# Performance work log

Hardware: AMD Instinct MI355X
Metric: run time of the kernel (lower is better)

## Reference

```python
import jax, jax.numpy as jnp
import numpy as np

DIM = 1024
N_HEADS = 16
HEAD_DIM = DIM // N_HEADS


def setup_inputs() -> dict:
    key = jax.random.key(0)
    k_x, k_wqkv, k_bqkv, k_wp, k_bp = jax.random.split(key, 5)
    s = 1.0 / np.sqrt(DIM)
    return {
        "x": jax.random.normal(k_x, (2, 2048, DIM), dtype=jnp.float32),
        "w_qkv": jax.random.uniform(k_wqkv, (3 * DIM, DIM), minval=-s, maxval=s, dtype=jnp.float32),
        "b_qkv": jax.random.uniform(k_bqkv, (3 * DIM,), minval=-s, maxval=s, dtype=jnp.float32),
        "w_proj": jax.random.uniform(k_wp, (DIM, DIM), minval=-s, maxval=s, dtype=jnp.float32),
        "b_proj": jax.random.uniform(k_bp, (DIM,), minval=-s, maxval=s, dtype=jnp.float32),
    }


def reference(x, w_qkv, b_qkv, w_proj, b_proj):
    B, S, D = x.shape
    H, Hd = N_HEADS, HEAD_DIM
    scale = jnp.asarray(Hd, x.dtype) ** 0.5
    qkv = x @ w_qkv.T + b_qkv                      # [B, S, 3D]
    q, k, v = jnp.split(qkv, 3, axis=-1)
    # [B, S, D] -> [B, H, S, Hd]
    q = q.reshape(B, S, H, Hd).transpose(0, 2, 1, 3)
    k = k.reshape(B, S, H, Hd).transpose(0, 2, 1, 3)
    v = v.reshape(B, S, H, Hd).transpose(0, 2, 1, 3)
    attn = jnp.einsum("bhqd,bhkd->bhqk", q, k) / scale
    attn = jax.nn.softmax(attn, axis=-1)
    out = jnp.einsum("bhqk,bhkd->bhqd", attn, v)   # [B, H, S, Hd]
    out = out.transpose(0, 2, 1, 3).reshape(B, S, D)
    return out @ w_proj.T + b_proj
```

## Files before the change

### kernel.cpp

```cpp
#include <hip/hip_runtime.h>

typedef __bf16 bf16;
typedef __bf16 bf16x4 __attribute__((ext_vector_type(4)));
typedef __bf16 bf16x8 __attribute__((ext_vector_type(8)));
typedef float f32x4 __attribute__((ext_vector_type(4)));
typedef float f32x16 __attribute__((ext_vector_type(16)));

#define DIMD 1024
#define NHEAD 16
#define HDIM 64
#define BATCH 2
#define SEQ 2048
#define MTOT (BATCH*SEQ)

#define EXP2F(x) __builtin_amdgcn_exp2f(x)

#define OFF_XB (0ull)
#define OFF_OB (0ull)
#define OFF_VT (8ull<<20)
#define OFF_WP (8ull<<20)

__device__ __forceinline__ void g2l16(const void* g, void* l) {
  __builtin_amdgcn_global_load_lds(
      (const __attribute__((address_space(1))) void*)g,
      (__attribute__((address_space(3))) void*)l,
      16, 0, 0);
}

__device__ __forceinline__ bf16x8 cvt8(float4 a, float4 b) {
  bf16x8 r = { (bf16)a.x, (bf16)a.y, (bf16)a.z, (bf16)a.w,
               (bf16)b.x, (bf16)b.y, (bf16)b.z, (bf16)b.w };
  return r;
}

__global__ __launch_bounds__(256) void cvt_kernel(const float* __restrict__ in,
                                                  bf16* __restrict__ out, int n4) {
  int i = blockIdx.x * blockDim.x + threadIdx.x;
  if (i < n4) {
    float4 v = ((const float4*)in)[i];
    bf16x4 o = { (bf16)v.x, (bf16)v.y, (bf16)v.z, (bf16)v.w };
    ((bf16x4*)out)[i] = o;
  }
}

__global__ __launch_bounds__(256, 3) void gemm_qkv(
    const bf16* __restrict__ A, const float* __restrict__ W,
    const float* __restrict__ bias,
    bf16* __restrict__ Qb, bf16* __restrict__ Kb, bf16* __restrict__ Vt)
{
  __shared__ bf16 lA[2][128 * 32];
  __shared__ bf16 lB[2][128 * 32];
  const int tid = threadIdx.x;
  const int wave = tid >> 6, lane = tid & 63;
  const int l15 = lane & 15, quad = lane >> 4;
  const int wm = wave >> 1, wn = wave & 1;
  const int tm = blockIdx.y * 128, tn = blockIdx.x * 128;

  f32x4 acc[4][4] = {};

  const int srow = tid >> 2, sch = (tid & 3) * 8;
  const bf16*  ga = &A[(size_t)(tm + srow) * DIMD + sch];
  const float* gb = &W[(size_t)(tn + srow) * DIMD + sch];

  g2l16(ga,                     &lA[0][wave * 512]);
  g2l16(ga + (size_t)64 * DIMD, &lA[0][2048 + wave * 512]);
  float4 bv0 = ((const float4*)gb)[0], bv1 = ((const float4*)gb)[1];
  float4 bv2 = ((const float4*)(gb + (size_t)64 * DIMD))[0],
         bv3 = ((const float4*)(gb + (size_t)64 * DIMD))[1];

  for (int kt = 0; kt < 32; kt++) {
    bf16* sB = lB[kt & 1];
    *(bf16x8*)&sB[srow * 32 + sch]        = cvt8(bv0, bv1);
    *(bf16x8*)&sB[(64 + srow) * 32 + sch] = cvt8(bv2, bv3);
    __syncthreads();

    if (kt < 31) {
      const int kn = (kt + 1) * 32;
      bf16* nA = lA[(kt + 1) & 1];
      g2l16(ga + kn,                     &nA[wave * 512]);
      g2l16(ga + kn + (size_t)64 * DIMD, &nA[2048 + wave * 512]);
      const float* gbn = gb + kn;
      bv0 = ((const float4*)gbn)[0]; bv1 = ((const float4*)gbn)[1];
      bv2 = ((const float4*)(gbn + (size_t)64 * DIMD))[0];
      bv3 = ((const float4*)(gbn + (size_t)64 * DIMD))[1];
    }

    const bf16* sA = lA[kt & 1];
    bf16x8 af[4], bfr[4];
#pragma unroll
    for (int i = 0; i < 4; i++)
      af[i] = *(const bf16x8*)&sA[(wm * 64 + i * 16 + l15) * 32 + quad * 8];
#pragma unroll
    for (int i = 0; i < 4; i++)
      bfr[i] = *(const bf16x8*)&sB[(wn * 64 + i * 16 + l15) * 32 + quad * 8];
#pragma unroll
    for (int i = 0; i < 4; i++)
#pragma unroll
      for (int j = 0; j < 4; j++)
        acc[i][j] = __builtin_amdgcn_mfma_f32_16x16x32_bf16(af[i], bfr[j], acc[i][j], 0, 0, 0);
  }

  const int sel = tn >> 10;
#pragma unroll
  for (int j = 0; j < 4; j++) {
    const int n = tn + wn * 64 + j * 16 + l15;
    const float bv = bias[n];
    const int d = n & 1023, h = d >> 6, hd = d & 63;
#pragma unroll
    for (int i = 0; i < 4; i++) {
      const int mbase = tm + wm * 64 + i * 16 + quad * 4;
      const int b = mbase >> 11, s0 = mbase & 2047;
      const int bh = b * NHEAD + h;
      if (sel == 2) {
        bf16x4 vv = { (bf16)(acc[i][j][0] + bv), (bf16)(acc[i][j][1] + bv),
                      (bf16)(acc[i][j][2] + bv), (bf16)(acc[i][j][3] + bv) };
        *(bf16x4*)&Vt[((size_t)bh * HDIM + hd) * SEQ + s0] = vv;
      } else {
#pragma unroll
        for (int r = 0; r < 4; r++) {
          float v = acc[i][j][r] + bv;
          if (sel == 0)
            Qb[((size_t)bh * SEQ + s0 + r) * HDIM + hd] = (bf16)(v * 0.18033688f);
          else
            Kb[((size_t)bh * SEQ + s0 + r) * HDIM + hd] = (bf16)v;
        }
      }
    }
  }
}

__global__ __launch_bounds__(256, 2) void gemm_proj(
    const bf16* __restrict__ A, const bf16* __restrict__ Bt,
    const float* __restrict__ bias, float* __restrict__ out)
{
  __shared__ bf16 lA[2][64 * 32];
  __shared__ bf16 lB[2][128 * 32];
  const int tid = threadIdx.x;
  const int wave = tid >> 6, lane = tid & 63;
  const int l15 = lane & 15, quad = lane >> 4;
  const int tm = blockIdx.y * 64, tn = blockIdx.x * 128;

  f32x4 acc[4][2] = {};

  const int srow = tid >> 2, sch = (tid & 3) * 8;
  const bf16* ga = &A[(size_t)(tm + srow) * DIMD + sch];
  const bf16* gb = &Bt[(size_t)(tn + srow) * DIMD + sch];

  g2l16(ga,                     &lA[0][wave * 512]);
  g2l16(gb,                     &lB[0][wave * 512]);
  g2l16(gb + (size_t)64 * DIMD, &lB[0][2048 + wave * 512]);

  for (int kt = 0; kt < 32; kt++) {
    __syncthreads();

    if (kt < 31) {
      const int kn = (kt + 1) * 32;
      bf16* nA = lA[(kt + 1) & 1];
      bf16* nB = lB[(kt + 1) & 1];
      g2l16(ga + kn,                     &nA[wave * 512]);
      g2l16(gb + kn,                     &nB[wave * 512]);
      g2l16(gb + kn + (size_t)64 * DIMD, &nB[2048 + wave * 512]);
    }

    const bf16* sA = lA[kt & 1];
    const bf16* sB = lB[kt & 1];
    bf16x8 af[4], bfr[2];
#pragma unroll
    for (int i = 0; i < 4; i++)
      af[i] = *(const bf16x8*)&sA[(i * 16 + l15) * 32 + quad * 8];
#pragma unroll
    for (int j = 0; j < 2; j++)
      bfr[j] = *(const bf16x8*)&sB[(wave * 32 + j * 16 + l15) * 32 + quad * 8];
#pragma unroll
    for (int i = 0; i < 4; i++)
#pragma unroll
      for (int j = 0; j < 2; j++)
        acc[i][j] = __builtin_amdgcn_mfma_f32_16x16x32_bf16(af[i], bfr[j], acc[i][j], 0, 0, 0);
  }

#pragma unroll
  for (int j = 0; j < 2; j++) {
    const int n = tn + wave * 32 + j * 16 + l15;
    const float bv = bias[n];
#pragma unroll
    for (int i = 0; i < 4; i++) {
      const int mbase = tm + i * 16 + quad * 4;
#pragma unroll
      for (int r = 0; r < 4; r++)
        out[(size_t)(mbase + r) * DIMD + n] = acc[i][j][r] + bv;
    }
  }
}

#define LSTR 72
__global__ __launch_bounds__(256, 2) void attn_kernel(
    const bf16* __restrict__ Qb, const bf16* __restrict__ Kb,
    const bf16* __restrict__ Vt, bf16* __restrict__ Ob)
{
  __shared__ bf16 lKV[2][2][64 * LSTR];
  __shared__ bf16 lP[4][32 * LSTR];

  const int tid = threadIdx.x;
  const int wave = tid >> 6, lane = tid & 63;
  const int l31 = lane & 31, h = lane >> 5;
  const int xcd = blockIdx.x & 7, grp = blockIdx.x >> 3;
  const int bh = xcd + 8 * (grp & 3);
  const int qt = grp >> 2;

  const int qrow = qt * 128 + wave * 32 + l31;
  const bf16* qp = Qb + ((size_t)bh * SEQ + qrow) * HDIM + h * 8;
  bf16x8 qf[4];
#pragma unroll
  for (int c = 0; c < 4; c++) qf[c] = *(const bf16x8*)(qp + c * 16);

  const int srow = tid >> 3;
  const int sch = (tid & 7) * 8;
  const bf16* kg = Kb + ((size_t)bh * SEQ + srow) * HDIM + sch;
  const bf16* vg = Vt + ((size_t)bh * HDIM + srow) * SEQ + sch;

  uint4 kr0 = *(const uint4*)(kg);
  uint4 kr1 = *(const uint4*)(kg + 32 * HDIM);
  uint4 vr0 = *(const uint4*)(vg);
  uint4 vr1 = *(const uint4*)(vg + 32 * SEQ);

  bf16* pw = lP[wave];

  f32x16 o0 = {}, o1 = {};
  float mrow = -1e30f, lrow = 0.f;

  for (int kt = 0; kt < SEQ / 64; kt++) {
    bf16* sK = lKV[kt & 1][0];
    bf16* sV = lKV[kt & 1][1];
    *(uint4*)&sK[srow * LSTR + sch]        = kr0;
    *(uint4*)&sK[(32 + srow) * LSTR + sch] = kr1;
    *(uint4*)&sV[srow * LSTR + sch]        = vr0;
    *(uint4*)&sV[(32 + srow) * LSTR + sch] = vr1;
    __syncthreads();

    const int ktn = (kt + 1) & (SEQ / 64 - 1);
    kr0 = *(const uint4*)(kg + (size_t)ktn * 64 * HDIM);
    kr1 = *(const uint4*)(kg + (size_t)ktn * 64 * HDIM + 32 * HDIM);
    vr0 = *(const uint4*)(vg + ktn * 64);
    vr1 = *(const uint4*)(vg + ktn * 64 + 32 * SEQ);

    f32x16 s0 = {}, s1 = {};
#pragma unroll
    for (int c = 0; c < 4; c++) {
      bf16x8 k0 = *(const bf16x8*)&sK[l31 * LSTR + c * 16 + h * 8];
      bf16x8 k1 = *(const bf16x8*)&sK[(32 + l31) * LSTR + c * 16 + h * 8];
      s0 = __builtin_amdgcn_mfma_f32_32x32x16_bf16(k0, qf[c], s0, 0, 0, 0);
      s1 = __builtin_amdgcn_mfma_f32_32x32x16_bf16(k1, qf[c], s1, 0, 0, 0);
    }

    if (kt > 0) {
      const bf16* pV = lKV[(kt + 1) & 1][1];
#pragma unroll
      for (int c = 0; c < 4; c++) {
        bf16x8 pf = *(const bf16x8*)&pw[l31 * LSTR + c * 16 + h * 8];
        bf16x8 v0 = *(const bf16x8*)&pV[l31 * LSTR + c * 16 + h * 8];
        bf16x8 v1 = *(const bf16x8*)&pV[(32 + l31) * LSTR + c * 16 + h * 8];
        o0 = __builtin_amdgcn_mfma_f32_32x32x16_bf16(v0, pf, o0, 0, 0, 0);
        o1 = __builtin_amdgcn_mfma_f32_32x32x16_bf16(v1, pf, o1, 0, 0, 0);
      }
    }

    float mx = -1e30f;
#pragma unroll
    for (int r = 0; r < 16; r++) { mx = fmaxf(mx, s0[r]); mx = fmaxf(mx, s1[r]); }
    mx = fmaxf(mx, __shfl_xor(mx, 32, 64));
    const float nm = fmaxf(mrow, mx);
    const float alpha = EXP2F(mrow - nm);
    mrow = nm;

    float rs = 0.f;
#pragma unroll
    for (int r = 0; r < 16; r++) {
      const float p0 = EXP2F(s0[r] - nm);
      const float p1 = EXP2F(s1[r] - nm);
      s0[r] = p0; s1[r] = p1;
      rs += p0 + p1;
    }
    rs += __shfl_xor(rs, 32, 64);
    lrow = lrow * alpha + rs;

#pragma unroll
    for (int r = 0; r < 16; r++) { o0[r] *= alpha; o1[r] *= alpha; }

#pragma unroll
    for (int g = 0; g < 4; g++) {
      bf16x4 pa = { (bf16)s0[4*g], (bf16)s0[4*g+1], (bf16)s0[4*g+2], (bf16)s0[4*g+3] };
      bf16x4 pb = { (bf16)s1[4*g], (bf16)s1[4*g+1], (bf16)s1[4*g+2], (bf16)s1[4*g+3] };
      *(bf16x4*)&pw[l31 * LSTR + g * 8 + h * 4]      = pa;
      *(bf16x4*)&pw[l31 * LSTR + 32 + g * 8 + h * 4] = pb;
    }
  }

  {
    const bf16* pV = lKV[1][1];
#pragma unroll
    for (int c = 0; c < 4; c++) {
      bf16x8 pf = *(const bf16x8*)&pw[l31 * LSTR + c * 16 + h * 8];
      bf16x8 v0 = *(const bf16x8*)&pV[l31 * LSTR + c * 16 + h * 8];
      bf16x8 v1 = *(const bf16x8*)&pV[(32 + l31) * LSTR + c * 16 + h * 8];
      o0 = __builtin_amdgcn_mfma_f32_32x32x16_bf16(v0, pf, o0, 0, 0, 0);
      o1 = __builtin_amdgcn_mfma_f32_32x32x16_bf16(v1, pf, o1, 0, 0, 0);
    }
  }

  const int b = bh >> 4, head = bh & 15;
  const float inv = 1.f / lrow;
  const size_t base = ((size_t)b * SEQ + qrow) * DIMD + head * HDIM;
#pragma unroll
  for (int g = 0; g < 4; g++) {
    bf16x4 oa = { (bf16)(o0[4*g] * inv), (bf16)(o0[4*g+1] * inv),
                  (bf16)(o0[4*g+2] * inv), (bf16)(o0[4*g+3] * inv) };
    bf16x4 ob = { (bf16)(o1[4*g] * inv), (bf16)(o1[4*g+1] * inv),
                  (bf16)(o1[4*g+2] * inv), (bf16)(o1[4*g+3] * inv) };
    *(bf16x4*)&Ob[base + g * 8 + h * 4]      = oa;
    *(bf16x4*)&Ob[base + 32 + g * 8 + h * 4] = ob;
  }
}

extern "C" void kernel_launch(void* const* d_in, const int* in_sizes, int n_in,
                              void* d_out, int out_size, void* d_ws, size_t ws_size,
                              hipStream_t stream) {
  const float* x      = (const float*)d_in[0];
  const float* w_qkv  = (const float*)d_in[1];
  const float* b_qkv  = (const float*)d_in[2];
  const float* w_proj = (const float*)d_in[3];
  const float* b_proj = (const float*)d_in[4];
  float* out = (float*)d_out;
  char* ws = (char*)d_ws;

  bf16* Qb = (bf16*)d_out;
  bf16* Kb = (bf16*)d_out + (size_t)MTOT * DIMD;
  bf16* xb     = (bf16*)(ws + OFF_XB);
  bf16* Ob     = (bf16*)(ws + OFF_OB);
  bf16* Vt     = (bf16*)(ws + OFF_VT);
  bf16* wprojb = (bf16*)(ws + OFF_WP);

  cvt_kernel<<<(MTOT * DIMD / 4) / 256, 256, 0, stream>>>(x, xb, MTOT * DIMD / 4);
  gemm_qkv<<<dim3(24, 32), 256, 0, stream>>>(xb, w_qkv, b_qkv, Qb, Kb, Vt);
  attn_kernel<<<BATCH * NHEAD * (SEQ / 128), 256, 0, stream>>>(Qb, Kb, Vt, Ob);
  cvt_kernel<<<(DIMD * DIMD / 4) / 256, 256, 0, stream>>>(w_proj, wprojb, DIMD * DIMD / 4);
  gemm_proj<<<dim3(8, 64), 256, 0, stream>>>(Ob, wprojb, b_proj, out);
}
```

Baseline: 194.5 us.

## Load V fragments directly to registers, swizzle LDS, add lazy softmax rescale

The attention kernel stops staging V in shared memory. Each lane now loads its V^T MFMA fragments straight from global memory into registers one iteration ahead. K and P tiles move from padded LDS rows to an XOR-swizzled 128-byte layout to avoid bank conflicts, and MFMA sections are wrapped in s_setprio. Softmax rescaling is skipped unless the running max grows by more than 8 (log2 units), and the max and sum reductions become trees. This cuts LDS traffic and exp/multiply work but raises register pressure and global load latency exposure, and it may lose precision when rescaling is deferred.

```diff
diff --git a/kernel.cpp b/kernel.cpp
--- a/kernel.cpp
+++ b/kernel.cpp
@@ -192,13 +192,12 @@
   }
 }
 
-#define LSTR 72
 __global__ __launch_bounds__(256, 2) void attn_kernel(
     const bf16* __restrict__ Qb, const bf16* __restrict__ Kb,
     const bf16* __restrict__ Vt, bf16* __restrict__ Ob)
 {
-  __shared__ bf16 lKV[2][2][64 * LSTR];
-  __shared__ bf16 lP[4][32 * LSTR];
+  __shared__ bf16 lK[2][64 * 64];
+  __shared__ bf16 lP[4][32 * 64];
 
   const int tid = threadIdx.x;
   const int wave = tid >> 6, lane = tid & 63;
@@ -216,95 +215,103 @@
   const int srow = tid >> 3;
   const int sch = (tid & 7) * 8;
   const bf16* kg = Kb + ((size_t)bh * SEQ + srow) * HDIM + sch;
-  const bf16* vg = Vt + ((size_t)bh * HDIM + srow) * SEQ + sch;
-
   uint4 kr0 = *(const uint4*)(kg);
   uint4 kr1 = *(const uint4*)(kg + 32 * HDIM);
-  uint4 vr0 = *(const uint4*)(vg);
-  uint4 vr1 = *(const uint4*)(vg + 32 * SEQ);
-
-  bf16* pw = lP[wave];
+  const int swb = (sch * 2) ^ ((srow & 7) << 4);
+
+  const bf16* vg0 = Vt + ((size_t)bh * HDIM + l31) * SEQ + h * 8;
+  const bf16* vg1 = vg0 + (size_t)32 * SEQ;
+  bf16x8 vf0[4], vf1[4];
+
+  char* pw = (char*)lP[wave];
+  const int px = (l31 & 7) << 4;
 
   f32x16 o0 = {}, o1 = {};
   float mrow = -1e30f, lrow = 0.f;
 
   for (int kt = 0; kt < SEQ / 64; kt++) {
-    bf16* sK = lKV[kt & 1][0];
-    bf16* sV = lKV[kt & 1][1];
-    *(uint4*)&sK[srow * LSTR + sch]        = kr0;
-    *(uint4*)&sK[(32 + srow) * LSTR + sch] = kr1;
-    *(uint4*)&sV[srow * LSTR + sch]        = vr0;
-    *(uint4*)&sV[(32 + srow) * LSTR + sch] = vr1;
+    char* sK = (char*)lK[kt & 1];
+    *(uint4*)(sK + srow * 128 + swb)        = kr0;
+    *(uint4*)(sK + (32 + srow) * 128 + swb) = kr1;
     __syncthreads();
 
     const int ktn = (kt + 1) & (SEQ / 64 - 1);
     kr0 = *(const uint4*)(kg + (size_t)ktn * 64 * HDIM);
     kr1 = *(const uint4*)(kg + (size_t)ktn * 64 * HDIM + 32 * HDIM);
-    vr0 = *(const uint4*)(vg + ktn * 64);
-    vr1 = *(const uint4*)(vg + ktn * 64 + 32 * SEQ);
 
     f32x16 s0 = {}, s1 = {};
+    __builtin_amdgcn_s_setprio(1);
 #pragma unroll
     for (int c = 0; c < 4; c++) {
-      bf16x8 k0 = *(const bf16x8*)&sK[l31 * LSTR + c * 16 + h * 8];
-      bf16x8 k1 = *(const bf16x8*)&sK[(32 + l31) * LSTR + c * 16 + h * 8];
+      bf16x8 k0 = *(const bf16x8*)(sK + l31 * 128 + (((c * 32) + h * 16) ^ px));
+      bf16x8 k1 = *(const bf16x8*)(sK + (32 + l31) * 128 + (((c * 32) + h * 16) ^ px));
       s0 = __builtin_amdgcn_mfma_f32_32x32x16_bf16(k0, qf[c], s0, 0, 0, 0);
       s1 = __builtin_amdgcn_mfma_f32_32x32x16_bf16(k1, qf[c], s1, 0, 0, 0);
     }
 
     if (kt > 0) {
-      const bf16* pV = lKV[(kt + 1) & 1][1];
 #pragma unroll
       for (int c = 0; c < 4; c++) {
-        bf16x8 pf = *(const bf16x8*)&pw[l31 * LSTR + c * 16 + h * 8];
-        bf16x8 v0 = *(const bf16x8*)&pV[l31 * LSTR + c * 16 + h * 8];
-        bf16x8 v1 = *(const bf16x8*)&pV[(32 + l31) * LSTR + c * 16 + h * 8];
-        o0 = __builtin_amdgcn_mfma_f32_32x32x16_bf16(v0, pf, o0, 0, 0, 0);
-        o1 = __builtin_amdgcn_mfma_f32_32x32x16_bf16(v1, pf, o1, 0, 0, 0);
+        bf16x8 pf = *(const bf16x8*)(pw + l31 * 128 + (((c * 32) + h * 16) ^ px));
+        o0 = __builtin_amdgcn_mfma_f32_32x32x16_bf16(vf0[c], pf, o0, 0, 0, 0);
+        o1 = __builtin_amdgcn_mfma_f32_32x32x16_bf16(vf1[c], pf, o1, 0, 0, 0);
       }
     }
-
-    float mx = -1e30f;
-#pragma unroll
-    for (int r = 0; r < 16; r++) { mx = fmaxf(mx, s0[r]); mx = fmaxf(mx, s1[r]); }
+    __builtin_amdgcn_s_setprio(0);
+
+#pragma unroll
+    for (int c = 0; c < 4; c++) {
+      vf0[c] = *(const bf16x8*)(vg0 + (size_t)kt * 64 + c * 16);
+      vf1[c] = *(const bf16x8*)(vg1 + (size_t)kt * 64 + c * 16);
+    }
+
+    float a[16];
+#pragma unroll
+    for (int r = 0; r < 8; r++)
+      a[r] = fmaxf(fmaxf(s0[r], s0[r + 8]), fmaxf(s1[r], s1[r + 8]));
+#pragma unroll
+    for (int r = 0; r < 4; r++) a[r] = fmaxf(a[r], a[r + 4]);
+    float mx = fmaxf(fmaxf(a[0], a[1]), fmaxf(a[2], a[3]));
     mx = fmaxf(mx, __shfl_xor(mx, 32, 64));
-    const float nm = fmaxf(mrow, mx);
-    const float alpha = EXP2F(mrow - nm);
-    mrow = nm;
-
-    float rs = 0.f;
+
+    if (!__all(mx - mrow <= 8.0f)) {
+      const float nm = fmaxf(mrow, mx);
+      const float alpha = EXP2F(mrow - nm);
+      mrow = nm;
+      lrow *= alpha;
+#pragma unroll
+      for (int r = 0; r < 16; r++) { o0[r] *= alpha; o1[r] *= alpha; }
+    }
+
 #pragma unroll
     for (int r = 0; r < 16; r++) {
-      const float p0 = EXP2F(s0[r] - nm);
-      const float p1 = EXP2F(s1[r] - nm);
+      const float p0 = EXP2F(s0[r] - mrow);
+      const float p1 = EXP2F(s1[r] - mrow);
       s0[r] = p0; s1[r] = p1;
-      rs += p0 + p1;
-    }
+      a[r] = p0 + p1;
+    }
+#pragma unroll
+    for (int r = 0; r < 8; r++) a[r] += a[r + 8];
+#pragma unroll
+    for (int r = 0; r < 4; r++) a[r] += a[r + 4];
+    float rs = (a[0] + a[1]) + (a[2] + a[3]);
     rs += __shfl_xor(rs, 32, 64);
-    lrow = lrow * alpha + rs;
-
-#pragma unroll
-    for (int r = 0; r < 16; r++) { o0[r] *= alpha; o1[r] *= alpha; }
+    lrow += rs;
 
 #pragma unroll
     for (int g = 0; g < 4; g++) {
       bf16x4 pa = { (bf16)s0[4*g], (bf16)s0[4*g+1], (bf16)s0[4*g+2], (bf16)s0[4*g+3] };
       bf16x4 pb = { (bf16)s1[4*g], (bf16)s1[4*g+1], (bf16)s1[4*g+2], (bf16)s1[4*g+3] };
-      *(bf16x4*)&pw[l31 * LSTR + g * 8 + h * 4]      = pa;
-      *(bf16x4*)&pw[l31 * LSTR + 32 + g * 8 + h * 4] = pb;
-    }
-  }
-
-  {
-    const bf16* pV = lKV[1][1];
-#pragma unroll
-    for (int c = 0; c < 4; c++) {
-      bf16x8 pf = *(const bf16x8*)&pw[l31 * LSTR + c * 16 + h * 8];
-      bf16x8 v0 = *(const bf16x8*)&pV[l31 * LSTR + c * 16 + h * 8];
-      bf16x8 v1 = *(const bf16x8*)&pV[(32 + l31) * LSTR + c * 16 + h * 8];
-      o0 = __builtin_amdgcn_mfma_f32_32x32x16_bf16(v0, pf, o0, 0, 0, 0);
-      o1 = __builtin_amdgcn_mfma_f32_32x32x16_bf16(v1, pf, o1, 0, 0, 0);
-    }
+      *(bf16x4*)(pw + l31 * 128 + (((g * 16) + h * 8) ^ px))      = pa;
+      *(bf16x4*)(pw + l31 * 128 + ((64 + (g * 16) + h * 8) ^ px)) = pb;
+    }
+  }
+
+#pragma unroll
+  for (int c = 0; c < 4; c++) {
+    bf16x8 pf = *(const bf16x8*)(pw + l31 * 128 + (((c * 32) + h * 16) ^ px));
+    o0 = __builtin_amdgcn_mfma_f32_32x32x16_bf16(vf0[c], pf, o0, 0, 0, 0);
+    o1 = __builtin_amdgcn_mfma_f32_32x32x16_bf16(vf1[c], pf, o1, 0, 0, 0);
   }
 
   const int b = bh >> 4, head = bh & 15;
```

Result: slower. 209.0 us (+7.4%).
